# Performance work log

Hardware: AMD Instinct MI355X
Metric: run time of the kernel (lower is better)

The kernel has to match this reference:

```python
import jax, jax.numpy as jnp
import numpy as np
import math

B, S, E, A = 8, 2048, 1024, 1024
NEG = -1e20

def setup_inputs() -> dict:
    key = jax.random.key(0)
    ks = jax.random.split(key, 6)
    scale = 1.0 / math.sqrt(E)
    return {
        "q": jax.random.normal(ks[0], (B, S, E), dtype=jnp.float32),
        "k": jax.random.normal(ks[1], (B, S, E), dtype=jnp.float32),
        "v": jax.random.normal(ks[2], (B, S, E), dtype=jnp.float32),
        "mask_pad": jnp.ones((B, S, S), dtype=jnp.int32),
        "Wq": jax.random.normal(ks[3], (E, A), dtype=jnp.float32) * scale,
        "Wk": jax.random.normal(ks[4], (E, A), dtype=jnp.float32) * scale,
        "Wv": jax.random.normal(ks[5], (E, A), dtype=jnp.float32) * scale,
    }

def reference(q, k, v, mask_pad, Wq, Wk, Wv):
    att_dim = Wq.shape[1]
    qp = jnp.einsum('bse,ea->bsa', q, Wq)
    kp = jnp.einsum('bse,ea->bsa', k, Wk)
    vp = jnp.einsum('bse,ea->bsa', v, Wv)
    # scores: [B, S, S]
    qk = jnp.einsum('bqa,bka->bqk', qp, kp) / jnp.sqrt(jnp.float32(att_dim))
    qk = jnp.where(mask_pad == 0, NEG, qk)
    # causal: torch.tril zeros out upper triangle, then zeros -> -1e20 (faithful quirk)
    seq = qk.shape[1]
    tril = jnp.tril(jnp.ones((seq, seq), dtype=bool))
    qk = jnp.where(tril[None, :, :], qk, 0.0)
    qk = jnp.where(qk == 0.0, NEG, qk)
    att_w = jax.nn.softmax(qk, axis=2)  # dropout p=0 -> identity
    return jnp.einsum('bqk,bka->bqa', att_w, vp)
```

## Files before the change

kernel.cpp:

```cpp
#include <hip/hip_runtime.h>
#include <math.h>

typedef __bf16 bf16x8 __attribute__((ext_vector_type(8)));
typedef float  f32x4  __attribute__((ext_vector_type(4)));
typedef unsigned short u16x8 __attribute__((ext_vector_type(8)));

#define NEGF (-1e20f)

__device__ __forceinline__ unsigned short f2bf(float f) {
  union { float f; unsigned u; } x; x.f = f;
  unsigned r = x.u + 0x7fffu + ((x.u >> 16) & 1u);
  return (unsigned short)(r >> 16);
}
__device__ __forceinline__ unsigned short f2bfh(float f) {
  __bf16 h = (__bf16)f;
  return __builtin_bit_cast(unsigned short, h);
}
__device__ __forceinline__ float bf2f(unsigned short h) {
  union { unsigned u; float f; } x; x.u = ((unsigned)h) << 16;
  return x.f;
}

__device__ __forceinline__ void gl16(const void* g, void* l) {
  __builtin_amdgcn_global_load_lds(
      (const __attribute__((address_space(1))) unsigned int*)g,
      (__attribute__((address_space(3))) unsigned int*)l, 16, 0, 0);
}
__device__ __forceinline__ unsigned lds_addr(const void* p) {
  return (unsigned)(unsigned long long)(const __attribute__((address_space(3))) char*)p;
}

#define DSR(dst, off) asm volatile("ds_read_b128 %0, %1" : "=v"(dst) : "v"(off))
#define LGKM0 asm volatile("s_waitcnt lgkmcnt(0)" ::: "memory")
#define VMC0  asm volatile("s_waitcnt vmcnt(0)" ::: "memory")
#define SBAR  __builtin_amdgcn_s_barrier()
#define SCH0  __builtin_amdgcn_sched_barrier(0)

__global__ __launch_bounds__(256) void k_cvt3(
    const float* __restrict__ q, const float* __restrict__ k, const float* __restrict__ v,
    unsigned short* __restrict__ qo, unsigned short* __restrict__ ko, unsigned short* __restrict__ vo) {
  const float* in = (blockIdx.y == 0) ? q : (blockIdx.y == 1) ? k : v;
  unsigned short* out = (blockIdx.y == 0) ? qo : (blockIdx.y == 1) ? ko : vo;
  size_t i = ((size_t)blockIdx.x * 256 + threadIdx.x) * 16;
  const float4* p = (const float4*)(in + i);
  float4 a = p[0], b = p[1], c = p[2], d = p[3];
  u16x8 o0, o1;
  o0[0] = f2bfh(a.x); o0[1] = f2bfh(a.y); o0[2] = f2bfh(a.z); o0[3] = f2bfh(a.w);
  o0[4] = f2bfh(b.x); o0[5] = f2bfh(b.y); o0[6] = f2bfh(b.z); o0[7] = f2bfh(b.w);
  o1[0] = f2bfh(c.x); o1[1] = f2bfh(c.y); o1[2] = f2bfh(c.z); o1[3] = f2bfh(c.w);
  o1[4] = f2bfh(d.x); o1[5] = f2bfh(d.y); o1[6] = f2bfh(d.z); o1[7] = f2bfh(d.w);
  *(u16x8*)(out + i) = o0;
  *(u16x8*)(out + i + 8) = o1;
}

__global__ __launch_bounds__(256) void k_cvt_w3(
    const float* __restrict__ Wq, const float* __restrict__ Wk, const float* __restrict__ Wv,
    unsigned short* __restrict__ Tq, unsigned short* __restrict__ Tk, unsigned short* __restrict__ Tv) {
  const float* W = (blockIdx.z == 0) ? Wq : (blockIdx.z == 1) ? Wk : Wv;
  unsigned short* WT = (blockIdx.z == 0) ? Tq : (blockIdx.z == 1) ? Tk : Tv;
  __shared__ float t[32][33];
  const int tid = threadIdx.x;
  const int tx = tid & 31, ty = tid >> 5;
  const int e0 = blockIdx.y * 32, a0 = blockIdx.x * 32;
#pragma unroll
  for (int i = 0; i < 4; i++) {
    int el = ty + i * 8;
    t[el][tx] = W[(size_t)(e0 + el) * 1024 + a0 + tx];
  }
  __syncthreads();
#pragma unroll
  for (int i = 0; i < 4; i++) {
    int al = ty + i * 8;
    WT[(size_t)(a0 + al) * 1024 + e0 + tx] = f2bf(t[tx][al]);
  }
}

__global__ __launch_bounds__(256) void k_maskbits(const int* __restrict__ mask,
                                                  unsigned short* __restrict__ bits) {
  size_t t = (size_t)blockIdx.x * 256 + threadIdx.x;
  const int4* p = (const int4*)(mask + t * 16);
  int4 a = p[0], b = p[1], c = p[2], d = p[3];
  unsigned m = 0;
  m |= (a.x != 0) ? 1u : 0u;      m |= (a.y != 0) ? 2u : 0u;
  m |= (a.z != 0) ? 4u : 0u;      m |= (a.w != 0) ? 8u : 0u;
  m |= (b.x != 0) ? 16u : 0u;     m |= (b.y != 0) ? 32u : 0u;
  m |= (b.z != 0) ? 64u : 0u;     m |= (b.w != 0) ? 128u : 0u;
  m |= (c.x != 0) ? 256u : 0u;    m |= (c.y != 0) ? 512u : 0u;
  m |= (c.z != 0) ? 1024u : 0u;   m |= (c.w != 0) ? 2048u : 0u;
  m |= (d.x != 0) ? 4096u : 0u;   m |= (d.y != 0) ? 8192u : 0u;
  m |= (d.z != 0) ? 16384u : 0u;  m |= (d.w != 0) ? 32768u : 0u;
  bits[t] = (unsigned short)m;
}

__global__ __launch_bounds__(256) void k_zdiag(unsigned short* __restrict__ E) {
  const int R = blockIdx.x, b = blockIdx.y;
  unsigned short* base = E + (size_t)b * 2048 * 2048
                           + (size_t)(R * 256) * 2048 + (R * 256 + 128);
  const u16x8 z = {0, 0, 0, 0, 0, 0, 0, 0};
  for (int i = threadIdx.x; i < 2048; i += 256) {
    int row = i >> 4, c = (i & 15) * 8;
    *(u16x8*)(base + (size_t)row * 2048 + c) = z;
  }
}

__device__ __forceinline__ void gemm256_core(
    const unsigned short* __restrict__ A, int lda,
    const unsigned short* __restrict__ Bt, int ldb,
    int brow, int bcol, int NT,
    unsigned short* As0, unsigned short* Bs0,
    f32x4 (&acc)[8][4])
{
  const int tid = threadIdx.x, w = tid >> 6, l = tid & 63;
  const int wr = w >> 2, wc = w & 3;
  const int fr = l & 15, fq = l >> 4;
  const int hr = l >> 3;
  const int hc = ((l & 7) ^ hr) * 8;

  const unsigned short* ga = A + (size_t)(brow + w * 32 + hr) * lda + hc;
  const unsigned short* gb = Bt + (size_t)(bcol + w * 32 + hr) * ldb + hc;

  unsigned aA[8], aB[4];
#pragma unroll
  for (int m = 0; m < 8; m++) aA[m] = lds_addr(As0) + (unsigned)((wr * 128 + m * 16 + fr) * 128);
#pragma unroll
  for (int n = 0; n < 4; n++) aB[n] = lds_addr(Bs0) + (unsigned)((wc * 64 + n * 16 + fr) * 128);
  const unsigned ck0 = (unsigned)((fq ^ (fr & 7)) * 16);
  const unsigned ck1 = (unsigned)(((4 + fq) ^ (fr & 7)) * 16);

  auto stage = [&](int buf, int k0) {
#pragma unroll
    for (int i = 0; i < 4; i++) {
      gl16(ga + (size_t)(8 * i) * lda + k0, As0 + buf * (256 * 64) + (w * 32 + 8 * i) * 64);
      gl16(gb + (size_t)(8 * i) * ldb + k0, Bs0 + buf * (256 * 64) + (w * 32 + 8 * i) * 64);
    }
  };

  stage(0, 0);
  VMC0; SBAR;
  for (int t = 0; t < NT; ++t) {
    if (t + 1 < NT) stage((t + 1) & 1, (t + 1) << 6);
    const unsigned bo = (unsigned)((t & 1) * (256 * 64 * 2));
    u16x8 ar[8], br[4];
#pragma unroll
    for (int m = 0; m < 8; m++) DSR(ar[m], aA[m] + bo + ck0);
#pragma unroll
    for (int n = 0; n < 4; n++) DSR(br[n], aB[n] + bo + ck0);
    LGKM0; SCH0;
    __builtin_amdgcn_s_setprio(1);
#pragma unroll
    for (int m = 0; m < 8; m++)
#pragma unroll
      for (int n = 0; n < 4; n++)
        acc[m][n] = __builtin_amdgcn_mfma_f32_16x16x32_bf16(
            __builtin_bit_cast(bf16x8, ar[m]), __builtin_bit_cast(bf16x8, br[n]), acc[m][n], 0, 0, 0);
    __builtin_amdgcn_s_setprio(0);
    u16x8 ar2[8], br2[4];
#pragma unroll
    for (int m = 0; m < 8; m++) DSR(ar2[m], aA[m] + bo + ck1);
#pragma unroll
    for (int n = 0; n < 4; n++) DSR(br2[n], aB[n] + bo + ck1);
    LGKM0; SCH0;
    __builtin_amdgcn_s_setprio(1);
#pragma unroll
    for (int m = 0; m < 8; m++)
#pragma unroll
      for (int n = 0; n < 4; n++)
        acc[m][n] = __builtin_amdgcn_mfma_f32_16x16x32_bf16(
            __builtin_bit_cast(bf16x8, ar2[m]), __builtin_bit_cast(bf16x8, br2[n]), acc[m][n], 0, 0, 0);
    __builtin_amdgcn_s_setprio(0);
    SCH0;
    VMC0; SBAR;
  }
}

__global__ __launch_bounds__(512, 2) void k_proj256(
    const unsigned short* __restrict__ A, int lda,
    const unsigned short* __restrict__ Bt, int ldb,
    unsigned short* __restrict__ C, int ldc, float scale)
{
  const int nwg = gridDim.x * gridDim.y;
  int lin = blockIdx.y * gridDim.x + blockIdx.x;
  int swz = (lin & 7) * (nwg >> 3) + (lin >> 3);
  const int bx = swz % gridDim.x, by = swz / gridDim.x;
  const int brow = by * 256, bcol = bx * 256;

  __shared__ unsigned short As[2][256 * 64];
  __shared__ unsigned short Bs[2][256 * 64];
  const int tid = threadIdx.x, w = tid >> 6, l = tid & 63;
  const int wr = w >> 2, wc = w & 3;
  const int fr = l & 15, fq = l >> 4;

  f32x4 acc[8][4] = {};
  gemm256_core(A, lda, Bt, ldb, brow, bcol, 16, &As[0][0], &Bs[0][0], acc);

#pragma unroll
  for (int m = 0; m < 8; m++)
#pragma unroll
    for (int n = 0; n < 4; n++)
#pragma unroll
      for (int r = 0; r < 4; r++) {
        int rg = brow + wr * 128 + m * 16 + fq * 4 + r;
        int cg = bcol + wc * 64 + n * 16 + fr;
        C[(size_t)rg * ldc + cg] = f2bf(acc[m][n][r] * scale);
      }
}

__device__ __forceinline__ void tile128_gemm(
    const unsigned short* __restrict__ A, int lda,
    const unsigned short* __restrict__ Bt, int ldb,
    int brow, int bcol, int NT,
    unsigned short* AsBase, unsigned short* BsBase,
    int wr, int wc, int fr, int fq,
    f32x4 (&acc)[4][4])
{
  const int tid = threadIdx.x, wid = tid >> 6, l = tid & 63;
  const int sr = l >> 3;
  const int sc = ((l & 7) ^ sr) * 8;

  const unsigned short* ga = A + (size_t)(brow + wid * 32 + sr) * lda + sc;
  const unsigned short* gb = Bt + (size_t)(bcol + wid * 32 + sr) * ldb + sc;

  unsigned aA[4], aB[4];
#pragma unroll
  for (int m = 0; m < 4; m++) aA[m] = lds_addr(AsBase) + (unsigned)((wr * 64 + m * 16 + fr) * 128);
#pragma unroll
  for (int n = 0; n < 4; n++) aB[n] = lds_addr(BsBase) + (unsigned)((wc * 64 + n * 16 + fr) * 128);
  const unsigned ck0 = (unsigned)((fq ^ (fr & 7)) * 16);
  const unsigned ck1 = (unsigned)(((4 + fq) ^ (fr & 7)) * 16);

  auto stage = [&](int buf, int k0) {
    unsigned short* la = AsBase + buf * (128 * 64);
    unsigned short* lb = BsBase + buf * (128 * 64);
#pragma unroll
    for (int i = 0; i < 4; i++) {
      gl16(ga + (size_t)(8 * i) * lda + k0, la + (wid * 32 + 8 * i) * 64);
      gl16(gb + (size_t)(8 * i) * ldb + k0, lb + (wid * 32 + 8 * i) * 64);
    }
  };

  stage(0, 0);
  VMC0; SBAR;

  for (int t = 0; t < NT; ++t) {
    if (t + 1 < NT) stage((t + 1) & 1, (t + 1) << 6);
    const unsigned bo = (unsigned)((t & 1) * (128 * 64 * 2));
    u16x8 ar[4], br[4];
#pragma unroll
    for (int m = 0; m < 4; m++) DSR(ar[m], aA[m] + bo + ck0);
#pragma unroll
    for (int n = 0; n < 4; n++) DSR(br[n], aB[n] + bo + ck0);
    LGKM0; SCH0;
    __builtin_amdgcn_s_setprio(1);
#pragma unroll
    for (int m = 0; m < 4; m++)
#pragma unroll
      for (int n = 0; n < 4; n++)
        acc[m][n] = __builtin_amdgcn_mfma_f32_16x16x32_bf16(
            __builtin_bit_cast(bf16x8, ar[m]), __builtin_bit_cast(bf16x8, br[n]), acc[m][n], 0, 0, 0);
    __builtin_amdgcn_s_setprio(0);
    u16x8 ar2[4], br2[4];
#pragma unroll
    for (int m = 0; m < 4; m++) DSR(ar2[m], aA[m] + bo + ck1);
#pragma unroll
    for (int n = 0; n < 4; n++) DSR(br2[n], aB[n] + bo + ck1);
    LGKM0; SCH0;
    __builtin_amdgcn_s_setprio(1);
#pragma unroll
    for (int m = 0; m < 4; m++)
#pragma unroll
      for (int n = 0; n < 4; n++)
        acc[m][n] = __builtin_amdgcn_mfma_f32_16x16x32_bf16(
            __builtin_bit_cast(bf16x8, ar2[m]), __builtin_bit_cast(bf16x8, br2[n]), acc[m][n], 0, 0, 0);
    __builtin_amdgcn_s_setprio(0);
    SCH0;
    VMC0;
    SBAR;
  }
}

__global__ __launch_bounds__(256, 2) void k_scores(
    const unsigned short* __restrict__ QP,
    const unsigned short* __restrict__ KP,
    unsigned short* __restrict__ E,
    const unsigned short* __restrict__ maskbits,
    float* __restrict__ rowsum)
{
  int bid0 = blockIdx.x;
  int bid = (bid0 & 7) * 136 + (bid0 >> 3);
  const int b = bid / 136;
  int t0 = bid - b * 136;
  int by = (int)((sqrtf((float)(8 * t0 + 1)) - 1.0f) * 0.5f);
  if ((by + 1) * (by + 2) / 2 <= t0) by++;
  else if (by * (by + 1) / 2 > t0) by--;
  const int bx = t0 - (by * (by + 1)) / 2;
  const int brow = by * 128, bcol = bx * 128;

  const unsigned short* A  = QP + (size_t)b * (2048 * 1024);
  const unsigned short* Bt = KP + (size_t)b * (2048 * 1024);

  __shared__ unsigned short As[2][128 * 64];
  __shared__ unsigned short Bs[2][128 * 64];

  const int tid = threadIdx.x, wid = tid >> 6, lane = tid & 63;
  const int wr = wid >> 1, wc = wid & 1;
  const int fr = lane & 15, fq = lane >> 4;

  const unsigned short* bits = maskbits + (size_t)b * 2048 * 128;
  unsigned mbits[2] = {0u, 0u};
#pragma unroll
  for (int m = 0; m < 4; m++)
#pragma unroll
    for (int r = 0; r < 4; r++) {
      int qq = brow + wr * 64 + m * 16 + fq * 4 + r;
      unsigned long long mw =
          *(const unsigned long long*)(bits + (size_t)qq * 128 + ((bcol + wc * 64) >> 4));
#pragma unroll
      for (int n = 0; n < 4; n++) {
        int jj = (m << 4) | (n << 2) | r;
        unsigned bit = (unsigned)((mw >> (n * 16 + fr)) & 1ull);
        mbits[jj >> 5] |= bit << (jj & 31);
      }
    }
  asm volatile("" ::: "memory");

  f32x4 acc[4][4] = {};
  tile128_gemm(A, 1024, Bt, 1024, brow, bcol, 16, &As[0][0], &Bs[0][0],
               wr, wc, fr, fq, acc);

  unsigned short* Cb = E + (size_t)b * 2048 * 2048;
  float* rs = rowsum + (size_t)b * 2048;
#pragma unroll
  for (int m = 0; m < 4; m++)
#pragma unroll
    for (int r = 0; r < 4; r++) {
      int qq = brow + wr * 64 + m * 16 + fq * 4 + r;
      float se = 0.f;
#pragma unroll
      for (int n = 0; n < 4; n++) {
        int jj = (m << 4) | (n << 2) | r;
        int kk = bcol + wc * 64 + n * 16 + fr;
        float s = acc[m][n][r];
        bool dead = !((mbits[jj >> 5] >> (jj & 31)) & 1u) || (kk > qq) || (s == 0.0f);
        float e = dead ? 0.f : __expf(s);
        se += e;
        Cb[(size_t)qq * 2048 + kk] = f2bf(e);
      }
      se += __shfl_xor(se, 1);
      se += __shfl_xor(se, 2);
      se += __shfl_xor(se, 4);
      se += __shfl_xor(se, 8);
      if (fr == 0) atomicAdd(&rs[qq], se);
    }
}

__global__ __launch_bounds__(512, 2) void k_pv256(
    const unsigned short* __restrict__ E,
    const unsigned short* __restrict__ VpT,
    const float* __restrict__ rowsum,
    float* __restrict__ Out)
{
  const int b = blockIdx.z;
  const int by = (int)(gridDim.y - 1 - blockIdx.y);
  const int bx = blockIdx.x;
  const int brow = by * 256, bcol = bx * 256;

  const unsigned short* A  = E + (size_t)b * 2048 * 2048;
  const unsigned short* Bt = VpT + (size_t)b * 2048;

  __shared__ unsigned short As[2][256 * 64];
  __shared__ unsigned short Bs[2][256 * 64];
  const int tid = threadIdx.x, w = tid >> 6, l = tid & 63;
  const int wr = w >> 2, wc = w & 3;
  const int fr = l & 15, fq = l >> 4;

  f32x4 acc[8][4] = {};
  const int NT = (brow + 256) >> 6;
  gemm256_core(A, 2048, Bt, 16384, brow, bcol, NT, &As[0][0], &Bs[0][0], acc);

  const float* rs = rowsum + (size_t)b * 2048;
  float* C = Out + (size_t)b * 2048 * 1024;
#pragma unroll
  for (int m = 0; m < 8; m++)
#pragma unroll
    for (int r = 0; r < 4; r++) {
      int rg = brow + wr * 128 + m * 16 + fq * 4 + r;
      float inv = 1.0f / rs[rg];
#pragma unroll
      for (int n = 0; n < 4; n++) {
        int cg = bcol + wc * 64 + n * 16 + fr;
        C[(size_t)rg * 1024 + cg] = acc[m][n][r] * inv;
      }
    }
}

extern "C" void kernel_launch(void* const* d_in, const int* in_sizes, int n_in,
                              void* d_out, int out_size, void* d_ws, size_t ws_size,
                              hipStream_t stream) {
  const float* q   = (const float*)d_in[0];
  const float* k   = (const float*)d_in[1];
  const float* v   = (const float*)d_in[2];
  const int*   msk = (const int*)d_in[3];
  const float* Wq  = (const float*)d_in[4];
  const float* Wk  = (const float*)d_in[5];
  const float* Wv  = (const float*)d_in[6];
  float* out = (float*)d_out;

  char* ws = (char*)d_ws;
  unsigned short* WqT = (unsigned short*)(ws + 0);
  unsigned short* WkT = (unsigned short*)(ws + 2097152);
  unsigned short* WvT = (unsigned short*)(ws + 4194304);
  unsigned short* qp  = (unsigned short*)(ws + 6291456);
  unsigned short* kp  = (unsigned short*)(ws + 39845888);
  unsigned short* vpT = (unsigned short*)(ws + 73400320);
  unsigned short* qbf = (unsigned short*)(ws + 106954752);
  unsigned short* kbf = (unsigned short*)(ws + 140509184);
  unsigned short* vbf = (unsigned short*)(ws + 174063616);
  unsigned short* E = (unsigned short*)(ws + 106954752);
  unsigned short* mbitsbuf = (unsigned short*)(ws + 207618048);
  float* rowsum = (float*)(ws + 211812352);

  dim3 blk(256), blk5(512);
  k_cvt3<<<dim3(4096, 3), blk, 0, stream>>>(q, k, v, qbf, kbf, vbf);
  k_cvt_w3<<<dim3(32, 32, 3), blk, 0, stream>>>(Wq, Wk, Wv, WqT, WkT, WvT);
  k_maskbits<<<dim3(8192), blk, 0, stream>>>(msk, mbitsbuf);
  hipMemsetAsync(rowsum, 0, 16384 * sizeof(float), stream);

  k_proj256<<<dim3(4, 64), blk5, 0, stream>>>(qbf, 1024, WqT, 1024, qp, 1024, 0.03125f);
  k_proj256<<<dim3(4, 64), blk5, 0, stream>>>(kbf, 1024, WkT, 1024, kp, 1024, 1.0f);
  k_proj256<<<dim3(64, 4), blk5, 0, stream>>>(WvT, 1024, vbf, 1024, vpT, 16384, 1.0f);

  k_zdiag<<<dim3(8, 8), blk, 0, stream>>>(E);

  k_scores<<<dim3(1088), blk, 0, stream>>>(qp, kp, E, mbitsbuf, rowsum);

  k_pv256<<<dim3(4, 8, 8), blk5, 0, stream>>>(E, vpT, rowsum, out);
  (void)in_sizes; (void)n_in; (void)out_size; (void)ws_size;
}
```

Measured before the change: 329.7 us.

## Fuse fp32-to-bf16 input conversion into projection GEMM loads

Removes the separate q/k/v fp32-to-bf16 conversion kernel. The projection GEMM now loads fp32 activations straight into registers, converts them to bf16 and writes them swizzled into LDS, while the bf16 weights still use async global-to-LDS loads. This saves writing and re-reading about 100MB of bf16 intermediates. In exchange the GEMM moves twice as many activation bytes from global memory and spends extra VALU and register pressure on conversion inside the pipelined main loop, using a partial vmcnt wait to overlap the next tile's loads.

```diff
diff --git a/kernel.cpp b/kernel.cpp
--- a/kernel.cpp
+++ b/kernel.cpp
@@ -16,10 +16,6 @@
   __bf16 h = (__bf16)f;
   return __builtin_bit_cast(unsigned short, h);
 }
-__device__ __forceinline__ float bf2f(unsigned short h) {
-  union { unsigned u; float f; } x; x.u = ((unsigned)h) << 16;
-  return x.f;
-}
 
 __device__ __forceinline__ void gl16(const void* g, void* l) {
   __builtin_amdgcn_global_load_lds(
@@ -33,25 +29,9 @@
 #define DSR(dst, off) asm volatile("ds_read_b128 %0, %1" : "=v"(dst) : "v"(off))
 #define LGKM0 asm volatile("s_waitcnt lgkmcnt(0)" ::: "memory")
 #define VMC0  asm volatile("s_waitcnt vmcnt(0)" ::: "memory")
+#define VMC8  asm volatile("s_waitcnt vmcnt(8)" ::: "memory")
 #define SBAR  __builtin_amdgcn_s_barrier()
 #define SCH0  __builtin_amdgcn_sched_barrier(0)
-
-__global__ __launch_bounds__(256) void k_cvt3(
-    const float* __restrict__ q, const float* __restrict__ k, const float* __restrict__ v,
-    unsigned short* __restrict__ qo, unsigned short* __restrict__ ko, unsigned short* __restrict__ vo) {
-  const float* in = (blockIdx.y == 0) ? q : (blockIdx.y == 1) ? k : v;
-  unsigned short* out = (blockIdx.y == 0) ? qo : (blockIdx.y == 1) ? ko : vo;
-  size_t i = ((size_t)blockIdx.x * 256 + threadIdx.x) * 16;
-  const float4* p = (const float4*)(in + i);
-  float4 a = p[0], b = p[1], c = p[2], d = p[3];
-  u16x8 o0, o1;
-  o0[0] = f2bfh(a.x); o0[1] = f2bfh(a.y); o0[2] = f2bfh(a.z); o0[3] = f2bfh(a.w);
-  o0[4] = f2bfh(b.x); o0[5] = f2bfh(b.y); o0[6] = f2bfh(b.z); o0[7] = f2bfh(b.w);
-  o1[0] = f2bfh(c.x); o1[1] = f2bfh(c.y); o1[2] = f2bfh(c.z); o1[3] = f2bfh(c.w);
-  o1[4] = f2bfh(d.x); o1[5] = f2bfh(d.y); o1[6] = f2bfh(d.z); o1[7] = f2bfh(d.w);
-  *(u16x8*)(out + i) = o0;
-  *(u16x8*)(out + i + 8) = o1;
-}
 
 __global__ __launch_bounds__(256) void k_cvt_w3(
     const float* __restrict__ Wq, const float* __restrict__ Wk, const float* __restrict__ Wv,
@@ -103,6 +83,155 @@
   }
 }
 
+template<int FSIDE>
+__global__ __launch_bounds__(512, 2) void k_projF(
+    const float* __restrict__ F, int ldf,
+    const unsigned short* __restrict__ H, int ldh,
+    unsigned short* __restrict__ C, int ldc, float scale)
+{
+  const int nwg = gridDim.x * gridDim.y;
+  int lin = blockIdx.y * gridDim.x + blockIdx.x;
+  int swz = (lin & 7) * (nwg >> 3) + (lin >> 3);
+  const int bx = swz % gridDim.x, by = swz / gridDim.x;
+  const int brow = by * 256, bcol = bx * 256;
+
+  __shared__ unsigned short As[2][256 * 64];
+  __shared__ unsigned short Bs[2][256 * 64];
+
+  const int tid = threadIdx.x, w = tid >> 6, l = tid & 63;
+  const int wr = w >> 2, wc = w & 3;
+  const int fr = l & 15, fq = l >> 4;
+
+  const int sr4 = tid >> 3;
+  const int scn = tid & 7;
+  const int hr = l >> 3;
+  const int hc = ((l & 7) ^ hr) * 8;
+
+  const int fbase = (FSIDE == 0) ? brow : bcol;
+  const int hbase = (FSIDE == 0) ? bcol : brow;
+  const float* gF = F + (size_t)(fbase + sr4 * 4) * ldf + scn * 8;
+  const unsigned short* gH = H + (size_t)(hbase + w * 32 + hr) * ldh + hc;
+
+  unsigned short* Fl = (FSIDE == 0) ? &As[0][0] : &Bs[0][0];
+  unsigned short* Hl = (FSIDE == 0) ? &Bs[0][0] : &As[0][0];
+
+  f32x4 acc[8][4] = {};
+
+  unsigned aA[8], aB[4];
+#pragma unroll
+  for (int m = 0; m < 8; m++) aA[m] = lds_addr(&As[0][0]) + (unsigned)((wr * 128 + m * 16 + fr) * 128);
+#pragma unroll
+  for (int n = 0; n < 4; n++) aB[n] = lds_addr(&Bs[0][0]) + (unsigned)((wc * 64 + n * 16 + fr) * 128);
+  const unsigned ck0 = (unsigned)((fq ^ (fr & 7)) * 16);
+  const unsigned ck1 = (unsigned)(((4 + fq) ^ (fr & 7)) * 16);
+
+  float4 f0[8], f1[8];
+
+#define LOADF(SET, K0) do {                                                    \
+    _Pragma("unroll")                                                          \
+    for (int i = 0; i < 4; i++) {                                              \
+      const float* p_ = gF + (size_t)i * ldf + (K0);                           \
+      SET[2 * i]     = *(const float4*)p_;                                     \
+      SET[2 * i + 1] = *(const float4*)(p_ + 4);                               \
+    } } while (0)
+
+#define WRITEF(SET, BUF) do {                                                  \
+    unsigned short* lb_ = Fl + (BUF) * (256 * 64);                             \
+    _Pragma("unroll")                                                          \
+    for (int i = 0; i < 4; i++) {                                              \
+      int row_ = sr4 * 4 + i;                                                  \
+      u16x8 o_;                                                                \
+      o_[0] = f2bfh(SET[2 * i].x);     o_[1] = f2bfh(SET[2 * i].y);            \
+      o_[2] = f2bfh(SET[2 * i].z);     o_[3] = f2bfh(SET[2 * i].w);            \
+      o_[4] = f2bfh(SET[2 * i + 1].x); o_[5] = f2bfh(SET[2 * i + 1].y);        \
+      o_[6] = f2bfh(SET[2 * i + 1].z); o_[7] = f2bfh(SET[2 * i + 1].w);        \
+      *(u16x8*)&lb_[row_ * 64 + ((scn ^ (row_ & 7)) * 8)] = o_;                \
+    } } while (0)
+
+#define STAGEH(BUF, K0) do {                                                   \
+    unsigned short* lb_ = Hl + (BUF) * (256 * 64);                             \
+    _Pragma("unroll")                                                          \
+    for (int i = 0; i < 4; i++)                                                \
+      gl16(gH + (size_t)(8 * i) * ldh + (K0), lb_ + (w * 32 + 8 * i) * 64);    \
+  } while (0)
+
+#define COMPUTE(BUF) do {                                                      \
+    const unsigned bo_ = (unsigned)((BUF) * (256 * 64 * 2));                   \
+    u16x8 ar_[8], br_[4];                                                      \
+    _Pragma("unroll")                                                          \
+    for (int m = 0; m < 8; m++) DSR(ar_[m], aA[m] + bo_ + ck0);                \
+    _Pragma("unroll")                                                          \
+    for (int n = 0; n < 4; n++) DSR(br_[n], aB[n] + bo_ + ck0);                \
+    LGKM0; SCH0;                                                               \
+    __builtin_amdgcn_s_setprio(1);                                             \
+    _Pragma("unroll")                                                          \
+    for (int m = 0; m < 8; m++)                                                \
+      _Pragma("unroll")                                                        \
+      for (int n = 0; n < 4; n++)                                              \
+        acc[m][n] = __builtin_amdgcn_mfma_f32_16x16x32_bf16(                   \
+            __builtin_bit_cast(bf16x8, ar_[m]), __builtin_bit_cast(bf16x8, br_[n]), acc[m][n], 0, 0, 0); \
+    __builtin_amdgcn_s_setprio(0);                                             \
+    u16x8 ar2_[8], br2_[4];                                                    \
+    _Pragma("unroll")                                                          \
+    for (int m = 0; m < 8; m++) DSR(ar2_[m], aA[m] + bo_ + ck1);               \
+    _Pragma("unroll")                                                          \
+    for (int n = 0; n < 4; n++) DSR(br2_[n], aB[n] + bo_ + ck1);               \
+    LGKM0; SCH0;                                                               \
+    __builtin_amdgcn_s_setprio(1);                                             \
+    _Pragma("unroll")                                                          \
+    for (int m = 0; m < 8; m++)                                                \
+      _Pragma("unroll")                                                        \
+      for (int n = 0; n < 4; n++)                                              \
+        acc[m][n] = __builtin_amdgcn_mfma_f32_16x16x32_bf16(                   \
+            __builtin_bit_cast(bf16x8, ar2_[m]), __builtin_bit_cast(bf16x8, br2_[n]), acc[m][n], 0, 0, 0); \
+    __builtin_amdgcn_s_setprio(0);                                             \
+    SCH0; } while (0)
+
+  LOADF(f0, 0);
+  STAGEH(0, 0);
+  LOADF(f1, 64);
+  VMC8;
+  WRITEF(f0, 0);
+  LGKM0; SBAR;
+
+  for (int t = 0; t < 14; t += 2) {
+    STAGEH(1, (t + 1) << 6);
+    LOADF(f0, (t + 2) << 6);
+    COMPUTE(0);
+    VMC8;
+    WRITEF(f1, 1);
+    LGKM0; SBAR;
+    STAGEH(0, (t + 2) << 6);
+    LOADF(f1, (t + 3) << 6);
+    COMPUTE(1);
+    VMC8;
+    WRITEF(f0, 0);
+    LGKM0; SBAR;
+  }
+  STAGEH(1, 15 << 6);
+  COMPUTE(0);
+  VMC0;
+  WRITEF(f1, 1);
+  LGKM0; SBAR;
+  COMPUTE(1);
+
+#undef LOADF
+#undef WRITEF
+#undef STAGEH
+#undef COMPUTE
+
+#pragma unroll
+  for (int m = 0; m < 8; m++)
+#pragma unroll
+    for (int n = 0; n < 4; n++)
+#pragma unroll
+      for (int r = 0; r < 4; r++) {
+        int rg = brow + wr * 128 + m * 16 + fq * 4 + r;
+        int cg = bcol + wc * 64 + n * 16 + fr;
+        C[(size_t)rg * ldc + cg] = f2bf(acc[m][n][r] * scale);
+      }
+}
+
 __device__ __forceinline__ void gemm256_core(
     const unsigned short* __restrict__ A, int lda,
     const unsigned short* __restrict__ Bt, int ldb,
@@ -171,38 +300,6 @@
     SCH0;
     VMC0; SBAR;
   }
-}
-
-__global__ __launch_bounds__(512, 2) void k_proj256(
-    const unsigned short* __restrict__ A, int lda,
-    const unsigned short* __restrict__ Bt, int ldb,
-    unsigned short* __restrict__ C, int ldc, float scale)
-{
-  const int nwg = gridDim.x * gridDim.y;
-  int lin = blockIdx.y * gridDim.x + blockIdx.x;
-  int swz = (lin & 7) * (nwg >> 3) + (lin >> 3);
-  const int bx = swz % gridDim.x, by = swz / gridDim.x;
-  const int brow = by * 256, bcol = bx * 256;
-
-  __shared__ unsigned short As[2][256 * 64];
-  __shared__ unsigned short Bs[2][256 * 64];
-  const int tid = threadIdx.x, w = tid >> 6, l = tid & 63;
-  const int wr = w >> 2, wc = w & 3;
-  const int fr = l & 15, fq = l >> 4;
-
-  f32x4 acc[8][4] = {};
-  gemm256_core(A, lda, Bt, ldb, brow, bcol, 16, &As[0][0], &Bs[0][0], acc);
-
-#pragma unroll
-  for (int m = 0; m < 8; m++)
-#pragma unroll
-    for (int n = 0; n < 4; n++)
-#pragma unroll
-      for (int r = 0; r < 4; r++) {
-        int rg = brow + wr * 128 + m * 16 + fq * 4 + r;
-        int cg = bcol + wc * 64 + n * 16 + fr;
-        C[(size_t)rg * ldc + cg] = f2bf(acc[m][n][r] * scale);
-      }
 }
 
 __device__ __forceinline__ void tile128_gemm(
@@ -412,22 +509,18 @@
   unsigned short* qp  = (unsigned short*)(ws + 6291456);
   unsigned short* kp  = (unsigned short*)(ws + 39845888);
   unsigned short* vpT = (unsigned short*)(ws + 73400320);
-  unsigned short* qbf = (unsigned short*)(ws + 106954752);
-  unsigned short* kbf = (unsigned short*)(ws + 140509184);
-  unsigned short* vbf = (unsigned short*)(ws + 174063616);
-  unsigned short* E = (unsigned short*)(ws + 106954752);
+  unsigned short* E   = (unsigned short*)(ws + 106954752);
   unsigned short* mbitsbuf = (unsigned short*)(ws + 207618048);
   float* rowsum = (float*)(ws + 211812352);
 
   dim3 blk(256), blk5(512);
-  k_cvt3<<<dim3(4096, 3), blk, 0, stream>>>(q, k, v, qbf, kbf, vbf);
   k_cvt_w3<<<dim3(32, 32, 3), blk, 0, stream>>>(Wq, Wk, Wv, WqT, WkT, WvT);
   k_maskbits<<<dim3(8192), blk, 0, stream>>>(msk, mbitsbuf);
   hipMemsetAsync(rowsum, 0, 16384 * sizeof(float), stream);
 
-  k_proj256<<<dim3(4, 64), blk5, 0, stream>>>(qbf, 1024, WqT, 1024, qp, 1024, 0.03125f);
-  k_proj256<<<dim3(4, 64), blk5, 0, stream>>>(kbf, 1024, WkT, 1024, kp, 1024, 1.0f);
-  k_proj256<<<dim3(64, 4), blk5, 0, stream>>>(WvT, 1024, vbf, 1024, vpT, 16384, 1.0f);
+  k_projF<0><<<dim3(4, 64), blk5, 0, stream>>>(q, 1024, WqT, 1024, qp, 1024, 0.03125f);
+  k_projF<0><<<dim3(4, 64), blk5, 0, stream>>>(k, 1024, WkT, 1024, kp, 1024, 1.0f);
+  k_projF<1><<<dim3(64, 4), blk5, 0, stream>>>(v, 1024, WvT, 1024, vpT, 16384, 1.0f);
 
   k_zdiag<<<dim3(8, 8), blk, 0, stream>>>(E);
 
```

New measurement: 859.5 us. 2.61x slower.

## Load-balance causal PV GEMM by pairing short and long row blocks per workgroup

Applied to the files above, without the earlier changes.

The causal P·V kernel previously gave each workgroup one 256-row block, so work per block varied with row position. The new kernel has each workgroup process two row blocks (7-j and j), which evens out the number of K-tiles per workgroup. It narrows the column tile to 128, uses 32-wide K tiles with swizzled LDS staging and a double-buffered pipeline, and raises wave priority around the MFMAs. A sched_barrier is also added in the conversion kernel. The narrower tile lowers reuse per staged A tile, and the two phases run back to back inside one workgroup.

```diff
diff --git a/kernel.cpp b/kernel.cpp
--- a/kernel.cpp
+++ b/kernel.cpp
@@ -44,6 +44,7 @@
   size_t i = ((size_t)blockIdx.x * 256 + threadIdx.x) * 16;
   const float4* p = (const float4*)(in + i);
   float4 a = p[0], b = p[1], c = p[2], d = p[3];
+  SCH0;
   u16x8 o0, o1;
   o0[0] = f2bfh(a.x); o0[1] = f2bfh(a.y); o0[2] = f2bfh(a.z); o0[3] = f2bfh(a.w);
   o0[4] = f2bfh(b.x); o0[5] = f2bfh(b.y); o0[6] = f2bfh(b.z); o0[7] = f2bfh(b.w);
@@ -353,44 +354,100 @@
     }
 }
 
-__global__ __launch_bounds__(512, 2) void k_pv256(
+__global__ __launch_bounds__(512, 2) void k_pv_bal(
     const unsigned short* __restrict__ E,
     const unsigned short* __restrict__ VpT,
     const float* __restrict__ rowsum,
     float* __restrict__ Out)
 {
-  const int b = blockIdx.z;
-  const int by = (int)(gridDim.y - 1 - blockIdx.y);
-  const int bx = blockIdx.x;
-  const int brow = by * 256, bcol = bx * 256;
-
-  const unsigned short* A  = E + (size_t)b * 2048 * 2048;
-  const unsigned short* Bt = VpT + (size_t)b * 2048;
-
-  __shared__ unsigned short As[2][256 * 64];
-  __shared__ unsigned short Bs[2][256 * 64];
+  const int j = blockIdx.x, bxc = blockIdx.y, b = blockIdx.z;
+  const int bcol = bxc * 128;
+
+  const unsigned short* EA = E + (size_t)b * 2048 * 2048;
+  const unsigned short* VB = VpT + (size_t)b * 2048;
+  const float* rs = rowsum + (size_t)b * 2048;
+  float* C = Out + (size_t)b * 2048 * 1024;
+
+  __shared__ unsigned short Al[2][256 * 32];
+  __shared__ unsigned short Bl[2][128 * 32];
+
   const int tid = threadIdx.x, w = tid >> 6, l = tid & 63;
   const int wr = w >> 2, wc = w & 3;
   const int fr = l & 15, fq = l >> 4;
 
-  f32x4 acc[8][4] = {};
-  const int NT = (brow + 256) >> 6;
-  gemm256_core(A, 2048, Bt, 16384, brow, bcol, NT, &As[0][0], &Bs[0][0], acc);
-
-  const float* rs = rowsum + (size_t)b * 2048;
-  float* C = Out + (size_t)b * 2048 * 1024;
+  unsigned aA[8], aB[2];
 #pragma unroll
   for (int m = 0; m < 8; m++)
-#pragma unroll
-    for (int r = 0; r < 4; r++) {
-      int rg = brow + wr * 128 + m * 16 + fq * 4 + r;
-      float inv = 1.0f / rs[rg];
-#pragma unroll
-      for (int n = 0; n < 4; n++) {
-        int cg = bcol + wc * 64 + n * 16 + fr;
-        C[(size_t)rg * 1024 + cg] = acc[m][n][r] * inv;
+    aA[m] = lds_addr(&Al[0][0]) + (unsigned)((wr * 128 + m * 16 + fr) * 64);
+#pragma unroll
+  for (int n = 0; n < 2; n++)
+    aB[n] = lds_addr(&Bl[0][0]) + (unsigned)((wc * 32 + n * 16 + fr) * 64);
+  const unsigned ck = (unsigned)((fq ^ (fr & 3)) * 16);
+
+#pragma unroll
+  for (int p = 0; p < 2; ++p) {
+    const int by = (p == 0) ? (7 - j) : j;
+    const int brow = by * 256;
+    const int NT = (by + 1) * 8;
+
+    auto stage = [&](int buf, int k0) {
+#pragma unroll
+      for (int i = 0; i < 3; i++) {
+        int slot = tid + 512 * i;
+        int row = slot >> 2, ch = slot & 3;
+        if (row < 256) {
+          gl16(EA + (size_t)(brow + row) * 2048 + k0 + ((ch ^ (row & 3)) * 8),
+               &Al[0][0] + buf * (256 * 32) + slot * 8);
+        } else {
+          int rb = row - 256;
+          gl16(VB + (size_t)(bcol + rb) * 16384 + k0 + ((ch ^ (rb & 3)) * 8),
+               &Bl[0][0] + buf * (128 * 32) + (slot - 1024) * 8);
+        }
       }
+    };
+
+    f32x4 acc[8][2] = {};
+
+    stage(0, 0);
+    VMC0; SBAR;
+    for (int t = 0; t < NT; ++t) {
+      if (t + 1 < NT) stage((t + 1) & 1, (t + 1) << 5);
+      const unsigned boA = (unsigned)((t & 1) * (256 * 32 * 2));
+      const unsigned boB = (unsigned)((t & 1) * (128 * 32 * 2));
+      u16x8 ar[8], br[2];
+#pragma unroll
+      for (int m = 0; m < 8; m++) DSR(ar[m], aA[m] + boA + ck);
+#pragma unroll
+      for (int n = 0; n < 2; n++) DSR(br[n], aB[n] + boB + ck);
+      LGKM0; SCH0;
+      __builtin_amdgcn_s_setprio(1);
+#pragma unroll
+      for (int m = 0; m < 8; m++)
+#pragma unroll
+        for (int n = 0; n < 2; n++)
+          acc[m][n] = __builtin_amdgcn_mfma_f32_16x16x32_bf16(
+              __builtin_bit_cast(bf16x8, ar[m]), __builtin_bit_cast(bf16x8, br[n]),
+              acc[m][n], 0, 0, 0);
+      __builtin_amdgcn_s_setprio(0);
+      SCH0;
+      VMC0;
+      SBAR;
     }
+
+#pragma unroll
+    for (int m = 0; m < 8; m++)
+#pragma unroll
+      for (int r = 0; r < 4; r++) {
+        int rg = brow + wr * 128 + m * 16 + fq * 4 + r;
+        float inv = 1.0f / rs[rg];
+#pragma unroll
+        for (int n = 0; n < 2; n++) {
+          int cg = bcol + wc * 32 + n * 16 + fr;
+          C[(size_t)rg * 1024 + cg] = acc[m][n][r] * inv;
+        }
+      }
+    SBAR;
+  }
 }
 
 extern "C" void kernel_launch(void* const* d_in, const int* in_sizes, int n_in,
@@ -433,6 +490,6 @@
 
   k_scores<<<dim3(1088), blk, 0, stream>>>(qp, kp, E, mbitsbuf, rowsum);
 
-  k_pv256<<<dim3(4, 8, 8), blk5, 0, stream>>>(E, vpT, rowsum, out);
+  k_pv_bal<<<dim3(4, 8, 8), blk5, 0, stream>>>(E, vpT, rowsum, out);
   (void)in_sizes; (void)n_in; (void)out_size; (void)ws_size;
 }
```

After: 330.3 us. No clear change (+0.2%).
